# Kernel tuning notes

Hardware: AMD Instinct MI355X
Metric: run time of the kernel (lower is better)

Reference implementation:

```python
import jax, jax.numpy as jnp
import numpy as np

D_MODEL = 2048
N_HEADS = 4
IDX_DIM = 64
B, TQ, TK = 2, 4096, 4096


def setup_inputs() -> dict:
    key = jax.random.key(0)
    k1, k2, k3, k4, k5 = jax.random.split(key, 5)
    x_q = jax.random.normal(k1, (B, TQ, D_MODEL), dtype=jnp.float32)
    x_k = jax.random.normal(k2, (B, TK, D_MODEL), dtype=jnp.float32)
    scale = 1.0 / np.sqrt(D_MODEL)
    Wq = jax.random.normal(k3, (D_MODEL, N_HEADS * IDX_DIM), dtype=jnp.float32) * scale
    Ww = jax.random.normal(k4, (D_MODEL, N_HEADS), dtype=jnp.float32) * scale
    Wk = jax.random.normal(k5, (D_MODEL, IDX_DIM), dtype=jnp.float32) * scale
    return {"x_q": x_q, "x_k": x_k, "Wq": Wq, "Ww": Ww, "Wk": Wk}


def reference(x_q, x_k, Wq, Ww, Wk):
    Bq, Tq, _ = x_q.shape
    # q_I: (B, Tq, H, d_idx); w_I: (B, Tq, H); k_I: (B, Tk, d_idx)
    q_I = (x_q @ Wq).reshape(Bq, Tq, N_HEADS, IDX_DIM)
    w_I = x_q @ Ww
    k_I = x_k @ Wk
    # per-head dot scores: (B, H, Tq, Tk), key projection shared across heads
    dot = jnp.einsum("bqhd,bkd->bhqk", q_I, k_I)
    activated = jax.nn.relu(dot)
    # weighted sum over heads -> (B, Tq, Tk)
    index_scores = jnp.einsum("bhqk,bqh->bqk", activated, w_I)
    return index_scores
```

## Files before the change

### kernel.cpp

```cpp
#include <hip/hip_runtime.h>
#include <hip/hip_bf16.h>

#define DM 2048
#define NH 4
#define DI 64
#define TQS 4096
#define TKS 4096
#define BB 2

typedef __attribute__((ext_vector_type(4))) float f32x4;
typedef __attribute__((ext_vector_type(8))) short bf16x8;

__device__ __forceinline__ short f2bf(float f) {
  __hip_bfloat16 h = __float2bfloat16(f);
  return __builtin_bit_cast(short, h);
}

__device__ __forceinline__ bf16x8 cvt8(f32x4 a, f32x4 b) {
  bf16x8 r;
  r[0] = f2bf(a[0]); r[1] = f2bf(a[1]); r[2] = f2bf(a[2]); r[3] = f2bf(a[3]);
  r[4] = f2bf(b[0]); r[5] = f2bf(b[1]); r[6] = f2bf(b[2]); r[7] = f2bf(b[3]);
  return r;
}

__global__ __launch_bounds__(256) void transpose_qw(const float* __restrict__ Wq,
                                                    const float* __restrict__ Ww,
                                                    short* __restrict__ WT) {
  int idx = blockIdx.x * 256 + threadIdx.x;
  int n = idx >> 11, k = idx & 2047;
  float v = 0.f;
  if (n < 256) v = Wq[(size_t)k * 256 + n];
  else if (n < 260) v = Ww[(size_t)k * 4 + (n - 256)];
  WT[idx] = f2bf(v);
}

__global__ __launch_bounds__(256) void transpose_k(const float* __restrict__ Wk,
                                                   short* __restrict__ WT) {
  int idx = blockIdx.x * 256 + threadIdx.x;
  int n = idx >> 11, k = idx & 2047;
  WT[idx] = f2bf(Wk[(size_t)k * 64 + n]);
}

template <int NJ, bool QP>
__device__ __forceinline__ void proj_body(const float* __restrict__ X,
                                          const short* __restrict__ WT,
                                          short* __restrict__ O,
                                          float* __restrict__ wI, int blk) {
  const int tid = threadIdx.x;
  const int wave = tid >> 6, lane = tid & 63;
  const int l15 = lane & 15, quad = lane >> 4;
  const int m0 = blk * 64;
  const int ldo = QP ? 256 : 64;

  int jt[NJ];
#pragma unroll
  for (int jj = 0; jj < NJ; ++jj) jt[jj] = QP ? (jj < 4 ? jj * 4 + wave : 16 + wave) : wave;

  const float* xbase = X + (size_t)(m0 + l15) * DM + quad * 8;
  const short* wb[NJ];
#pragma unroll
  for (int jj = 0; jj < NJ; ++jj) wb[jj] = WT + (size_t)(jt[jj] * 16 + l15) * DM + quad * 8;

  const f32x4 z = {0.f, 0.f, 0.f, 0.f};
  f32x4 acc[NJ][4];
#pragma unroll
  for (int jj = 0; jj < NJ; ++jj)
#pragma unroll
    for (int i = 0; i < 4; ++i) acc[jj][i] = z;

  f32x4 araw[2][4][2];
#pragma unroll
  for (int i = 0; i < 4; ++i) {
    araw[0][i][0] = *(const f32x4*)(xbase + i * 16 * DM);
    araw[0][i][1] = *(const f32x4*)(xbase + i * 16 * DM + 4);
    araw[1][i][0] = *(const f32x4*)(xbase + i * 16 * DM + 32);
    araw[1][i][1] = *(const f32x4*)(xbase + i * 16 * DM + 36);
  }
  bf16x8 bcur[NJ];
#pragma unroll
  for (int jj = 0; jj < NJ; ++jj) bcur[jj] = *(const bf16x8*)wb[jj];

#pragma unroll 2
  for (int ks = 0; ks < 64; ++ks) {
    const int s = ks & 1;
    bf16x8 abf[4];
#pragma unroll
    for (int i = 0; i < 4; ++i) abf[i] = cvt8(araw[s][i][0], araw[s][i][1]);
    if (ks < 62) {
      const float* xp = xbase + (ks + 2) * 32;
#pragma unroll
      for (int i = 0; i < 4; ++i) {
        araw[s][i][0] = *(const f32x4*)(xp + i * 16 * DM);
        araw[s][i][1] = *(const f32x4*)(xp + i * 16 * DM + 4);
      }
    }
    bf16x8 bnxt[NJ];
    if (ks < 63) {
#pragma unroll
      for (int jj = 0; jj < NJ; ++jj) bnxt[jj] = *(const bf16x8*)(wb[jj] + (ks + 1) * 32);
    } else {
#pragma unroll
      for (int jj = 0; jj < NJ; ++jj) bnxt[jj] = bcur[jj];
    }
#pragma unroll
    for (int jj = 0; jj < NJ; ++jj)
#pragma unroll
      for (int i = 0; i < 4; ++i)
        acc[jj][i] = __builtin_amdgcn_mfma_f32_16x16x32_bf16(abf[i], bcur[jj],
                                                             acc[jj][i], 0, 0, 0);
#pragma unroll
    for (int jj = 0; jj < NJ; ++jj) bcur[jj] = bnxt[jj];
  }

#pragma unroll
  for (int jj = 0; jj < NJ; ++jj) {
    if (QP && jt[jj] >= 16) {
      if (jt[jj] == 16 && l15 < 4) {
#pragma unroll
        for (int i = 0; i < 4; ++i)
#pragma unroll
          for (int r = 0; r < 4; ++r)
            wI[(size_t)(m0 + i * 16 + quad * 4 + r) * NH + l15] = acc[jj][i][r];
      }
    } else {
#pragma unroll
      for (int i = 0; i < 4; ++i)
#pragma unroll
        for (int r = 0; r < 4; ++r)
          O[(size_t)(m0 + i * 16 + quad * 4 + r) * ldo + jt[jj] * 16 + l15] =
              f2bf(acc[jj][i][r]);
    }
  }
}

__global__ __launch_bounds__(256, 1) void proj_fused(const float* __restrict__ xq,
                                                     const float* __restrict__ xk,
                                                     const short* __restrict__ WqwT,
                                                     const short* __restrict__ WkT,
                                                     short* __restrict__ qb,
                                                     short* __restrict__ kb,
                                                     float* __restrict__ wIb) {
  if (blockIdx.x < 128)
    proj_body<5, true>(xq, WqwT, qb, wIb, blockIdx.x);
  else
    proj_body<1, false>(xk, WkT, kb, nullptr, blockIdx.x - 128);
}

__global__ __launch_bounds__(256, 2) void score_kernel(const short* __restrict__ qb,
                                                       const short* __restrict__ kb,
                                                       const float* __restrict__ wI,
                                                       float* __restrict__ out) {
  const int b = blockIdx.z;
  const int qt = blockIdx.y;
  const int kt = blockIdx.x;
  const int tid = threadIdx.x;
  const int wave = tid >> 6, lane = tid & 63;
  const int wm = wave >> 1, wn = wave & 1;
  const int l15 = lane & 15, quad = lane >> 4;

  bf16x8 bf[4][2];
  {
    const short* kbase =
        kb + (size_t)(b * TKS + kt * 128 + wn * 64 + l15) * DI + quad * 8;
#pragma unroll
    for (int j = 0; j < 4; ++j)
#pragma unroll
      for (int ks = 0; ks < 2; ++ks)
        bf[j][ks] = *(const bf16x8*)(kbase + j * 16 * DI + ks * 32);
  }

  const f32x4 z = {0.f, 0.f, 0.f, 0.f};
  f32x4 facc[4][4];
#pragma unroll
  for (int i = 0; i < 4; ++i)
#pragma unroll
    for (int j = 0; j < 4; ++j) facc[i][j] = z;

  const short* qbase =
      qb + (size_t)(b * TQS + qt * 128 + wm * 64 + l15) * (NH * DI) + quad * 8;
  const float* wbase = wI + (size_t)(b * TQS + qt * 128 + wm * 64 + quad * 4) * NH;

  bf16x8 af[2][4][2];
#pragma unroll
  for (int i = 0; i < 4; ++i)
#pragma unroll
    for (int ks = 0; ks < 2; ++ks)
      af[0][i][ks] = *(const bf16x8*)(qbase + i * 16 * (NH * DI) + ks * 32);

#pragma unroll
  for (int h = 0; h < NH; ++h) {
    if (h < NH - 1) {
#pragma unroll
      for (int i = 0; i < 4; ++i)
#pragma unroll
        for (int ks = 0; ks < 2; ++ks)
          af[(h + 1) & 1][i][ks] =
              *(const bf16x8*)(qbase + (h + 1) * DI + i * 16 * (NH * DI) + ks * 32);
    }

    f32x4 acc[4][4];
#pragma unroll
    for (int i = 0; i < 4; ++i)
#pragma unroll
      for (int j = 0; j < 4; ++j) acc[i][j] = z;

#pragma unroll
    for (int ks = 0; ks < 2; ++ks)
#pragma unroll
      for (int i = 0; i < 4; ++i)
#pragma unroll
        for (int j = 0; j < 4; ++j)
          acc[i][j] = __builtin_amdgcn_mfma_f32_16x16x32_bf16(
              af[h & 1][i][ks], bf[j][ks], acc[i][j], 0, 0, 0);

#pragma unroll
    for (int i = 0; i < 4; ++i) {
      float wv[4];
#pragma unroll
      for (int r = 0; r < 4; ++r) wv[r] = wbase[(i * 16 + r) * NH + h];
#pragma unroll
      for (int j = 0; j < 4; ++j)
#pragma unroll
        for (int r = 0; r < 4; ++r)
          facc[i][j][r] += wv[r] * fmaxf(acc[i][j][r], 0.f);
    }
  }

  float* obase = out + (size_t)b * TQS * TKS +
                 (size_t)(qt * 128 + wm * 64 + quad * 4) * TKS + kt * 128 + wn * 64 + l15;
#pragma unroll
  for (int i = 0; i < 4; ++i)
#pragma unroll
    for (int r = 0; r < 4; ++r)
#pragma unroll
      for (int j = 0; j < 4; ++j)
        __builtin_nontemporal_store(facc[i][j][r],
                                    &obase[(size_t)(i * 16 + r) * TKS + j * 16]);
}

extern "C" void kernel_launch(void* const* d_in, const int* in_sizes, int n_in,
                              void* d_out, int out_size, void* d_ws, size_t ws_size,
                              hipStream_t stream) {
  const float* x_q = (const float*)d_in[0];
  const float* x_k = (const float*)d_in[1];
  const float* Wq  = (const float*)d_in[2];
  const float* Ww  = (const float*)d_in[3];
  const float* Wk  = (const float*)d_in[4];
  float* out = (float*)d_out;

  char* ws = (char*)d_ws;
  short* qbuf = (short*)(ws);
  short* kbuf = (short*)(ws + (4u << 20));
  float* wIb  = (float*)(ws + (5u << 20));
  short* WqwT = (short*)(ws + (5u << 20) + (128u << 10));
  short* WkT  = (short*)(ws + (7u << 20));

  transpose_qw<<<(320 * 2048) / 256, 256, 0, stream>>>(Wq, Ww, WqwT);
  transpose_k<<<(64 * 2048) / 256, 256, 0, stream>>>(Wk, WkT);

  proj_fused<<<256, 256, 0, stream>>>(x_q, x_k, WqwT, WkT, qbuf, kbuf, wIb);

  score_kernel<<<dim3(TKS / 128, TQS / 128, BB), 256, 0, stream>>>(qbuf, kbuf, wIb, out);
}
```

Measured before the change: 343.5 us.

## Split projection into 16-row tiles across many more blocks

Restructures the fused projection kernel so that each wave computes a 16-row by 64-column output tile. Previously each wave handled 64 rows with up to five column tiles, and only 256 blocks were launched. The new launch uses 615 blocks of 320 threads with a higher occupancy bound, meant to fill the GPU's compute units better during the projection phase. The cost is reuse: each x row is now read by every wave instead of being amortized across four row tiles per weight load, which raises global and cache traffic. Waves in the w tile do mostly wasted MFMA work.

```diff
diff --git a/kernel.cpp b/kernel.cpp
--- a/kernel.cpp
+++ b/kernel.cpp
@@ -7,6 +7,7 @@
 #define TQS 4096
 #define TKS 4096
 #define BB 2
+#define MROWS 8192
 
 typedef __attribute__((ext_vector_type(4))) float f32x4;
 typedef __attribute__((ext_vector_type(8))) short bf16x8;
@@ -41,109 +42,84 @@
   WT[idx] = f2bf(Wk[(size_t)k * 64 + n]);
 }
 
-template <int NJ, bool QP>
-__device__ __forceinline__ void proj_body(const float* __restrict__ X,
-                                          const short* __restrict__ WT,
-                                          short* __restrict__ O,
-                                          float* __restrict__ wI, int blk) {
-  const int tid = threadIdx.x;
-  const int wave = tid >> 6, lane = tid & 63;
+__device__ __forceinline__ void proj16(const float* __restrict__ X,
+                                       const short* __restrict__ WT,
+                                       short* __restrict__ O,
+                                       float* __restrict__ wI,
+                                       int m0, int nt, int ldo, bool wtile) {
+  const int lane = threadIdx.x & 63;
   const int l15 = lane & 15, quad = lane >> 4;
-  const int m0 = blk * 64;
-  const int ldo = QP ? 256 : 64;
-
-  int jt[NJ];
-#pragma unroll
-  for (int jj = 0; jj < NJ; ++jj) jt[jj] = QP ? (jj < 4 ? jj * 4 + wave : 16 + wave) : wave;
-
-  const float* xbase = X + (size_t)(m0 + l15) * DM + quad * 8;
-  const short* wb[NJ];
-#pragma unroll
-  for (int jj = 0; jj < NJ; ++jj) wb[jj] = WT + (size_t)(jt[jj] * 16 + l15) * DM + quad * 8;
+
+  const float* xrow = X + (size_t)(m0 + l15) * DM + quad * 8;
+  const short* wrow = WT + (size_t)(nt * 64 + l15) * DM + quad * 8;
 
   const f32x4 z = {0.f, 0.f, 0.f, 0.f};
-  f32x4 acc[NJ][4];
-#pragma unroll
-  for (int jj = 0; jj < NJ; ++jj)
-#pragma unroll
-    for (int i = 0; i < 4; ++i) acc[jj][i] = z;
-
-  f32x4 araw[2][4][2];
-#pragma unroll
-  for (int i = 0; i < 4; ++i) {
-    araw[0][i][0] = *(const f32x4*)(xbase + i * 16 * DM);
-    araw[0][i][1] = *(const f32x4*)(xbase + i * 16 * DM + 4);
-    araw[1][i][0] = *(const f32x4*)(xbase + i * 16 * DM + 32);
-    araw[1][i][1] = *(const f32x4*)(xbase + i * 16 * DM + 36);
-  }
-  bf16x8 bcur[NJ];
-#pragma unroll
-  for (int jj = 0; jj < NJ; ++jj) bcur[jj] = *(const bf16x8*)wb[jj];
+  f32x4 acc[4];
+#pragma unroll
+  for (int j = 0; j < 4; ++j) acc[j] = z;
+
+  f32x4 a0 = *(const f32x4*)xrow;
+  f32x4 a1 = *(const f32x4*)(xrow + 4);
+  bf16x8 bcur[4];
+#pragma unroll
+  for (int j = 0; j < 4; ++j) bcur[j] = *(const bf16x8*)(wrow + (size_t)j * 16 * DM);
 
 #pragma unroll 2
-  for (int ks = 0; ks < 64; ++ks) {
-    const int s = ks & 1;
-    bf16x8 abf[4];
-#pragma unroll
-    for (int i = 0; i < 4; ++i) abf[i] = cvt8(araw[s][i][0], araw[s][i][1]);
-    if (ks < 62) {
-      const float* xp = xbase + (ks + 2) * 32;
-#pragma unroll
-      for (int i = 0; i < 4; ++i) {
-        araw[s][i][0] = *(const f32x4*)(xp + i * 16 * DM);
-        araw[s][i][1] = *(const f32x4*)(xp + i * 16 * DM + 4);
-      }
-    }
-    bf16x8 bnxt[NJ];
-    if (ks < 63) {
-#pragma unroll
-      for (int jj = 0; jj < NJ; ++jj) bnxt[jj] = *(const bf16x8*)(wb[jj] + (ks + 1) * 32);
+  for (int ks = 0; ks < DM / 32; ++ks) {
+    f32x4 an0 = a0, an1 = a1;
+    bf16x8 bnxt[4];
+    if (ks < DM / 32 - 1) {
+      const float* xp = xrow + (ks + 1) * 32;
+      an0 = *(const f32x4*)xp;
+      an1 = *(const f32x4*)(xp + 4);
+#pragma unroll
+      for (int j = 0; j < 4; ++j)
+        bnxt[j] = *(const bf16x8*)(wrow + (size_t)j * 16 * DM + (ks + 1) * 32);
     } else {
 #pragma unroll
-      for (int jj = 0; jj < NJ; ++jj) bnxt[jj] = bcur[jj];
-    }
-#pragma unroll
-    for (int jj = 0; jj < NJ; ++jj)
-#pragma unroll
-      for (int i = 0; i < 4; ++i)
-        acc[jj][i] = __builtin_amdgcn_mfma_f32_16x16x32_bf16(abf[i], bcur[jj],
-                                                             acc[jj][i], 0, 0, 0);
-#pragma unroll
-    for (int jj = 0; jj < NJ; ++jj) bcur[jj] = bnxt[jj];
-  }
-
-#pragma unroll
-  for (int jj = 0; jj < NJ; ++jj) {
-    if (QP && jt[jj] >= 16) {
-      if (jt[jj] == 16 && l15 < 4) {
-#pragma unroll
-        for (int i = 0; i < 4; ++i)
-#pragma unroll
-          for (int r = 0; r < 4; ++r)
-            wI[(size_t)(m0 + i * 16 + quad * 4 + r) * NH + l15] = acc[jj][i][r];
-      }
-    } else {
-#pragma unroll
-      for (int i = 0; i < 4; ++i)
-#pragma unroll
-        for (int r = 0; r < 4; ++r)
-          O[(size_t)(m0 + i * 16 + quad * 4 + r) * ldo + jt[jj] * 16 + l15] =
-              f2bf(acc[jj][i][r]);
-    }
-  }
-}
-
-__global__ __launch_bounds__(256, 1) void proj_fused(const float* __restrict__ xq,
+      for (int j = 0; j < 4; ++j) bnxt[j] = bcur[j];
+    }
+    bf16x8 abf = cvt8(a0, a1);
+#pragma unroll
+    for (int j = 0; j < 4; ++j)
+      acc[j] = __builtin_amdgcn_mfma_f32_16x16x32_bf16(abf, bcur[j], acc[j], 0, 0, 0);
+    a0 = an0; a1 = an1;
+#pragma unroll
+    for (int j = 0; j < 4; ++j) bcur[j] = bnxt[j];
+  }
+
+  if (wtile) {
+    if (l15 < 4) {
+#pragma unroll
+      for (int r = 0; r < 4; ++r)
+        wI[(size_t)(m0 + quad * 4 + r) * NH + l15] = acc[0][r];
+    }
+  } else {
+#pragma unroll
+    for (int j = 0; j < 4; ++j)
+#pragma unroll
+      for (int r = 0; r < 4; ++r)
+        O[(size_t)(m0 + quad * 4 + r) * ldo + nt * 64 + j * 16 + l15] =
+            f2bf(acc[j][r]);
+  }
+}
+
+__global__ __launch_bounds__(320, 4) void proj_fused(const float* __restrict__ xq,
                                                      const float* __restrict__ xk,
                                                      const short* __restrict__ WqwT,
                                                      const short* __restrict__ WkT,
                                                      short* __restrict__ qb,
                                                      short* __restrict__ kb,
                                                      float* __restrict__ wIb) {
-  if (blockIdx.x < 128)
-    proj_body<5, true>(xq, WqwT, qb, wIb, blockIdx.x);
-  else
-    proj_body<1, false>(xk, WkT, kb, nullptr, blockIdx.x - 128);
+  const int wave = threadIdx.x >> 6;
+  if (blockIdx.x < 512) {
+    const int m0 = blockIdx.x * 16;
+    proj16(xq, WqwT, qb, wIb, m0, wave, 256, wave == 4);
+  } else {
+    const int m0 = (blockIdx.x - 512) * 80 + wave * 16;
+    if (m0 >= MROWS) return;
+    proj16(xk, WkT, kb, nullptr, m0, 0, 64, false);
+  }
 }
 
 __global__ __launch_bounds__(256, 2) void score_kernel(const short* __restrict__ qb,
@@ -258,7 +234,7 @@
   transpose_qw<<<(320 * 2048) / 256, 256, 0, stream>>>(Wq, Ww, WqwT);
   transpose_k<<<(64 * 2048) / 256, 256, 0, stream>>>(Wk, WkT);
 
-  proj_fused<<<256, 256, 0, stream>>>(x_q, x_k, WqwT, WkT, qbuf, kbuf, wIb);
+  proj_fused<<<512 + 103, 320, 0, stream>>>(x_q, x_k, WqwT, WkT, qbuf, kbuf, wIb);
 
   score_kernel<<<dim3(TKS / 128, TQS / 128, BB), 256, 0, stream>>>(qbuf, kbuf, wIb, out);
 }
```

After: 423.8 us. +23.4%, slower.
